# Performance work log

Measured on AMD Instinct MI355X. Metric: run time of the kernel, lower is better.

Reference implementation:

```python
import jax, jax.numpy as jnp
import numpy as np

N_NODES = 8000
N_EDGES = 64000
HEADS = 8
OUT_C = 512
NEG_SLOPE = 0.2
EPS = 1e-16


def setup_inputs() -> dict:
    key = jax.random.key(0)
    ks = jax.random.split(key, 8)
    x = jax.random.normal(ks[0], (N_NODES, 128), dtype=jnp.float32)
    edge_index = jax.random.randint(ks[1], (2, N_EDGES), 0, N_NODES, dtype=jnp.int64)
    W_gat = jax.random.normal(ks[2], (128, HEADS * OUT_C), dtype=jnp.float32) * 0.05
    b_gat = jax.random.normal(ks[3], (HEADS * OUT_C,), dtype=jnp.float32) * 0.05
    att_src = jax.random.normal(ks[4], (HEADS, OUT_C), dtype=jnp.float32) * 0.05
    att_dst = jax.random.normal(ks[5], (HEADS, OUT_C), dtype=jnp.float32) * 0.05
    W_lin = jax.random.normal(ks[6], (HEADS * OUT_C, 512), dtype=jnp.float32) * 0.02
    b_lin = jax.random.normal(ks[7], (512,), dtype=jnp.float32) * 0.02
    return {"x": x, "edge_index": edge_index, "W_gat": W_gat, "b_gat": b_gat,
            "att_src": att_src, "att_dst": att_dst, "W_lin": W_lin, "b_lin": b_lin}


def reference(x, edge_index, W_gat, b_gat, att_src, att_dst, W_lin, b_lin):
    N = x.shape[0]
    # shared linear projection (PyG GATConv single-tensor input): [N, H, C]
    h = (x @ W_gat).reshape(N, HEADS, OUT_C)
    # add self loops (PyG default add_self_loops=True)
    loop = jnp.arange(N, dtype=edge_index.dtype)
    src = jnp.concatenate([edge_index[0], loop])  # source j
    dst = jnp.concatenate([edge_index[1], loop])  # destination i
    # per-node attention logits: [N, H]
    a_src = jnp.einsum('nhc,hc->nh', h, att_src)
    a_dst = jnp.einsum('nhc,hc->nh', h, att_dst)
    # edge logits, leaky relu
    e = jax.nn.leaky_relu(a_src[src] + a_dst[dst], NEG_SLOPE)  # [E, H]
    # softmax over edges sharing a destination
    emax = jax.ops.segment_max(e, dst, num_segments=N)
    ez = jnp.exp(e - emax[dst])
    denom = jax.ops.segment_sum(ez, dst, num_segments=N)
    alpha = ez / (denom[dst] + EPS)  # [E, H]
    # weighted scatter-add of source features
    msg = h[src] * alpha[:, :, None]  # [E, H, C]
    agg = jax.ops.segment_sum(msg, dst, num_segments=N)  # [N, H, C]
    gat_out = agg.reshape(N, HEADS * OUT_C) + b_gat
    return gat_out @ W_lin + b_lin
```

## Files before the change

kernel.cpp:

```cpp
#include <hip/hip_runtime.h>
#include <hip/hip_bf16.h>
#include <type_traits>

#define NN   8000
#define NE   64000
#define NE2  72000
#define NH   8
#define OC   512
#define HC   4096
#define KIN  128
#define NOUT 512
#define YW   1024
#define MAXDEG 64
#define NEG_SLOPE 0.2f

using bf16 = __hip_bfloat16;
typedef float  f32x4  __attribute__((ext_vector_type(4)));
typedef __bf16 bf16x8 __attribute__((ext_vector_type(8)));

static __device__ __forceinline__ void gld_lds16(const bf16* g, bf16* l){
    __builtin_amdgcn_global_load_lds(
        (const __attribute__((address_space(1))) unsigned int*)g,
        (__attribute__((address_space(3))) unsigned int*)l, 16, 0, 0);
}

struct Acc24 { f32x4 a[2][4]; };

static __device__ __forceinline__ void gemm64x128(
    const bf16* __restrict__ A, int lda, const bf16* __restrict__ BT, int ldb,
    int K, bf16* sA, bf16* sB, int tid, Acc24& acc)
{
    const int lane = tid & 63;
    const int w    = tid >> 6;
    const int wm   = w >> 1, wn = w & 1;
    const int m16  = lane & 15, q = lane >> 4;
    const int rA = tid >> 2,  kA = (tid & 3) * 8;
    const int cB0 = tid, cB1 = 256 + tid;
    const int rB0 = cB0 >> 2, kB0 = (cB0 & 3) * 8;
    const int rB1 = cB1 >> 2, kB1 = (cB1 & 3) * 8;
    const size_t gA  = (size_t)rA  * lda + kA;
    const size_t gB0 = (size_t)rB0 * ldb + kB0;
    const size_t gB1 = (size_t)rB1 * ldb + kB1;

    #pragma unroll
    for (int i=0;i<2;++i)
        #pragma unroll
        for (int j=0;j<4;++j)
            #pragma unroll
            for (int r=0;r<4;++r) acc.a[i][j][r] = 0.f;

    gld_lds16(A  + gA,  sA + tid*8);
    gld_lds16(BT + gB0, sB + cB0*8);
    gld_lds16(BT + gB1, sB + cB1*8);
    __syncthreads();

    const int nIter = K / 32;
    for (int it = 0; it < nIter; ++it){
        const int cur = it & 1, nxt = cur ^ 1;
        bf16x8 af[2], bfr[4];
        #pragma unroll
        for (int i=0;i<2;++i)
            af[i]  = *(const bf16x8*)(const void*)(sA + cur*64*32 + ((wm*32 + i*16 + m16)*32 + q*8));
        #pragma unroll
        for (int j=0;j<4;++j)
            bfr[j] = *(const bf16x8*)(const void*)(sB + cur*128*32 + ((wn*64 + j*16 + m16)*32 + q*8));
        if (it + 1 < nIter){
            int ko = (it+1) * 32;
            gld_lds16(A  + gA  + ko, sA + nxt*64*32 + tid*8);
            gld_lds16(BT + gB0 + ko, sB + nxt*128*32 + cB0*8);
            gld_lds16(BT + gB1 + ko, sB + nxt*128*32 + cB1*8);
        }
        #pragma unroll
        for (int i=0;i<2;++i)
            #pragma unroll
            for (int j=0;j<4;++j)
                acc.a[i][j] = __builtin_amdgcn_mfma_f32_16x16x32_bf16(af[i], bfr[j], acc.a[i][j], 0, 0, 0);
        __syncthreads();
    }
}

#define VSRC_NB   128
#define BEFF_BASE 128
#define CNT_BASE  160
#define PHA_NB    442

__global__ __launch_bounds__(256) void k_phaseA(
    const float* __restrict__ b_gat, const float* __restrict__ W_gat,
    const float* __restrict__ att_src, const float* __restrict__ att_dst,
    const float* __restrict__ W_lin,
    const int* __restrict__ eidx,
    bf16* __restrict__ Wg, float* __restrict__ v,
    float* __restrict__ b_eff,
    int* __restrict__ cursors, int* __restrict__ esrc)
{
    const int bid = blockIdx.x;
    const int tid = threadIdx.x;

    if (bid < VSRC_NB){
        int k = bid;
        int lane = tid & 63, g = tid >> 6;
        for (int hh = g; hh < NH; hh += 4){
            const float* wp = W_gat + (size_t)k*HC + hh*OC;
            bf16*        wb = Wg    + (size_t)k*HC + hh*OC;
            const float* as = att_src + hh*OC;
            const float* ad = att_dst + hh*OC;
            float ss = 0.f, sd = 0.f;
            #pragma unroll
            for (int c0=0; c0<OC; c0+=64){
                float wv = wp[c0+lane];
                wb[c0+lane] = __float2bfloat16(wv);
                ss = fmaf(wv, as[c0+lane], ss);
                sd = fmaf(wv, ad[c0+lane], sd);
            }
            #pragma unroll
            for (int off=32; off; off>>=1){
                ss += __shfl_down(ss, off);
                sd += __shfl_down(sd, off);
            }
            if (lane == 0){
                v[k*16 + hh]     = ss;
                v[k*16 + 8 + hh] = sd;
            }
        }
    } else if (bid < CNT_BASE){
        int b = bid - BEFF_BASE;
        int o = tid * 2;
        const float* bg = b_gat + b*128;
        const float* wl = W_lin + (size_t)b*128*NOUT + o;
        float a0 = 0.f, a1 = 0.f;
        #pragma unroll 4
        for (int c=0; c<128; ++c){
            float bv = bg[c];
            float2 wv = *(const float2*)(wl + (size_t)c*NOUT);
            a0 = fmaf(bv, wv.x, a0);
            a1 = fmaf(bv, wv.y, a1);
        }
        atomicAdd(b_eff + o,     a0);
        atomicAdd(b_eff + o + 1, a1);
    } else {
        int e = (bid - CNT_BASE)*256 + tid;
        if (e < NE2){
            int src, dst;
            if (e < NE){ src = eidx[e]; dst = eidx[NE+e]; } else { src = dst = e - NE; }
            int pos = atomicAdd(&cursors[dst], 1);
            if (pos < MAXDEG) esrc[dst*MAXDEG + pos] = src;
        }
    }
}

#define PB_GEMM_NB 64
#define ATT_BASE   64
#define PHB_NB     564

__global__ __launch_bounds__(256) void k_phaseB(
    const bf16* __restrict__ Wg, const float* __restrict__ W_lin,
    bf16* __restrict__ WcT,
    const float* __restrict__ x, const float* __restrict__ v,
    float* __restrict__ a_src, float* __restrict__ a_dst)
{
    __shared__ __align__(16) char smem_raw[16*132*2*4];
    const int bid = blockIdx.x;
    const int tid = threadIdx.x;

    if (bid < PB_GEMM_NB){
        bf16* sA = (bf16*)smem_raw;
        bf16* sB = (bf16*)smem_raw + 64*32;

        const int head = bid >> 3;
        const int rem  = bid & 7;
        const int m0   = (rem >> 2) * 64;
        const int n0   = (rem & 3) * 128;
        const int lane = tid & 63;
        const int w = tid >> 6, wm = w >> 1, wn = w & 1;
        const int m16 = lane & 15, q = lane >> 4;

        const int rA = tid >> 2, kA = (tid & 3) * 8;
        const bf16* Abase = Wg + (size_t)(m0 + rA)*HC + head*OC + kA;

        f32x4 acc[2][4];
        #pragma unroll
        for (int i=0;i<2;++i)
            #pragma unroll
            for (int j=0;j<4;++j)
                #pragma unroll
                for (int r=0;r<4;++r) acc[i][j][r] = 0.f;

        for (int kc = 0; kc < OC; kc += 32){
            __syncthreads();
            gld_lds16(Abase + kc, sA + tid*8);
            #pragma unroll
            for (int u=0; u<4; ++u){
                int idx = tid*4 + u;
                int r    = idx >> 5;
                int gcol = (idx & 31) * 4;
                const float* src = W_lin + (size_t)(head*OC + kc + r)*NOUT + n0 + gcol;
                float4 vv = *(const float4*)src;
                sB[(gcol+0)*32 + r] = __float2bfloat16(vv.x);
                sB[(gcol+1)*32 + r] = __float2bfloat16(vv.y);
                sB[(gcol+2)*32 + r] = __float2bfloat16(vv.z);
                sB[(gcol+3)*32 + r] = __float2bfloat16(vv.w);
            }
            __syncthreads();
            bf16x8 af[2], bfr[4];
            #pragma unroll
            for (int i=0;i<2;++i)
                af[i]  = *(const bf16x8*)(const void*)(sA + ((wm*32 + i*16 + m16)*32 + q*8));
            #pragma unroll
            for (int j=0;j<4;++j)
                bfr[j] = *(const bf16x8*)(const void*)(sB + ((wn*64 + j*16 + m16)*32 + q*8));
            #pragma unroll
            for (int i=0;i<2;++i)
                #pragma unroll
                for (int j=0;j<4;++j)
                    acc[i][j] = __builtin_amdgcn_mfma_f32_16x16x32_bf16(af[i], bfr[j], acc[i][j], 0, 0, 0);
        }

        #pragma unroll
        for (int i=0;i<2;++i){
            int row_base = m0 + wm*32 + i*16 + q*4;
            #pragma unroll
            for (int j=0;j<4;++j){
                int col = n0 + wn*64 + j*16 + m16;
                ushort4 pk;
                bf16 b0 = __float2bfloat16(acc[i][j][0]);
                bf16 b1 = __float2bfloat16(acc[i][j][1]);
                bf16 b2 = __float2bfloat16(acc[i][j][2]);
                bf16 b3 = __float2bfloat16(acc[i][j][3]);
                pk.x = *(unsigned short*)&b0; pk.y = *(unsigned short*)&b1;
                pk.z = *(unsigned short*)&b2; pk.w = *(unsigned short*)&b3;
                *reinterpret_cast<ushort4*>(WcT + (size_t)col*YW + head*KIN + row_base) = pk;
            }
        }
        return;
    }

    float (*xs)[132] = (float(*)[132])smem_raw;
    float (*vt)[132] = (float(*)[132])(smem_raw + 16*132*4);
    int node0 = (bid - ATT_BASE) * 16;
    {
        const float* xg = x + (size_t)node0*KIN;
        int row = tid >> 4, co = (tid & 15) * 8;
        float4 v0 = *(const float4*)(xg + row*KIN + co);
        float4 v1 = *(const float4*)(xg + row*KIN + co + 4);
        *(float4*)&xs[row][co]     = v0;
        *(float4*)&xs[row][co + 4] = v1;
    }
    {
        int base = tid*8;
        #pragma unroll
        for (int j=0;j<8;++j){
            int idx = base + j;
            vt[idx & 15][idx >> 4] = v[idx];
        }
    }
    __syncthreads();
    int ln = tid >> 4, o = tid & 15;
    float acc = 0.f;
    #pragma unroll
    for (int k0=0;k0<KIN;k0+=4){
        float4 xv = *(const float4*)&xs[ln][k0];
        float4 vv = *(const float4*)&vt[o][k0];
        acc += xv.x*vv.x + xv.y*vv.y + xv.z*vv.z + xv.w*vv.w;
    }
    int node = node0 + ln;
    if (o < 8) a_src[node*NH + o]     = acc;
    else       a_dst[node*NH + o - 8] = acc;
}

__global__ __launch_bounds__(256) void k_agg(const int* __restrict__ cnts,
    const int* __restrict__ esrc, const float* __restrict__ a_src,
    const float* __restrict__ a_dst, const float* __restrict__ x,
    bf16* __restrict__ Y)
{
    int node = blockIdx.x*4 + (threadIdx.x >> 6);
    int lane = threadIdx.x & 63;
    int s0 = node*MAXDEG, s1 = s0 + cnts[node];
    int g = lane >> 3, h = lane & 7;
    float adl = a_dst[node*NH + h];
    float m = -1e30f, sum = 0.f;
    for (int e = s0 + g; e < s1; e += 8){
        float l = a_src[esrc[e]*NH + h] + adl;
        l = l > 0.f ? l : NEG_SLOPE*l;
        float mn = fmaxf(m, l);
        sum = sum*__expf(m - mn) + __expf(l - mn);
        m = mn;
    }
    #pragma unroll
    for (int d=8; d<64; d<<=1){
        float mo = __shfl_xor(m, d);
        float so = __shfl_xor(sum, d);
        float mn = fmaxf(m, mo);
        sum = sum*__expf(m - mn) + so*__expf(mo - mn);
        m = mn;
    }
    float inv = 1.f / (sum + 1e-16f);
    float acc[16];
    #pragma unroll
    for (int j=0;j<16;++j) acc[j] = 0.f;
    for (int s=s0; s<s1; ++s){
        int src = esrc[s];
        float wl = 0.f;
        if (lane < 8){
            float l = a_src[src*NH + lane] + adl;
            l = l > 0.f ? l : NEG_SLOPE*l;
            wl = __expf(l - m) * inv;
        }
        float2 xv = *(const float2*)(x + (size_t)src*KIN + lane*2);
        #pragma unroll
        for (int hh=0; hh<8; ++hh){
            float wh = __shfl(wl, hh);
            acc[hh*2]   = fmaf(wh, xv.x, acc[hh*2]);
            acc[hh*2+1] = fmaf(wh, xv.y, acc[hh*2+1]);
        }
    }
    bf16* yp = Y + (size_t)node*YW + lane*2;
    #pragma unroll
    for (int hh=0; hh<8; ++hh){
        bf16 b0 = __float2bfloat16(acc[hh*2]);
        bf16 b1 = __float2bfloat16(acc[hh*2+1]);
        ushort2 pk;
        pk.x = *(unsigned short*)&b0;
        pk.y = *(unsigned short*)&b1;
        *reinterpret_cast<ushort2*>(yp + hh*KIN) = pk;
    }
}

__global__ __launch_bounds__(256) void k_gemm64(
    const bf16* __restrict__ A, const bf16* __restrict__ BT,
    const float* __restrict__ b_eff, const float* __restrict__ b_lin,
    float* __restrict__ C)
{
    __shared__ __align__(16) char smem_raw[24576];
    bf16* sA = (bf16*)smem_raw;
    bf16* sB = (bf16*)(smem_raw + 8192);
    const int tid = threadIdx.x;
    int m0 = blockIdx.x * 64;
    int n0 = blockIdx.y * 128;
    Acc24 acc;
    gemm64x128(A + (size_t)m0*YW, YW, BT + (size_t)n0*YW, YW, YW, sA, sB, tid, acc);
    const int lane = tid & 63;
    const int w = tid >> 6, wm = w >> 1, wn = w & 1;
    const int m16 = lane & 15, q = lane >> 4;
    #pragma unroll
    for (int i=0;i<2;++i){
        int row_base = m0 + wm*32 + i*16 + q*4;
        #pragma unroll
        for (int j=0;j<4;++j){
            int col = n0 + wn*64 + j*16 + m16;
            float bval = b_eff[col] + b_lin[col];
            #pragma unroll
            for (int r=0;r<4;++r)
                C[(size_t)(row_base + r)*NOUT + col] = acc.a[i][j][r] + bval;
        }
    }
}

extern "C" void kernel_launch(void* const* d_in, const int* in_sizes, int n_in,
                              void* d_out, int out_size, void* d_ws, size_t ws_size,
                              hipStream_t stream)
{
    const float* x       = (const float*)d_in[0];
    const int*   eidx    = (const int*)  d_in[1];
    const float* W_gat   = (const float*)d_in[2];
    const float* b_gat   = (const float*)d_in[3];
    const float* att_src = (const float*)d_in[4];
    const float* att_dst = (const float*)d_in[5];
    const float* W_lin   = (const float*)d_in[6];
    const float* b_lin   = (const float*)d_in[7];
    float* out = (float*)d_out;

    char* p = (char*)d_ws;
    auto alloc = [&](size_t bytes){ void* r = (void*)p; p += (bytes + 255) & ~(size_t)255; return r; };
    bf16*  Wg     = (bf16*) alloc((size_t)KIN*HC*2);
    bf16*  WcT    = (bf16*) alloc((size_t)NOUT*YW*2);
    bf16*  Ybuf   = (bf16*) alloc((size_t)NN*YW*2);
    float* v      = (float*)alloc((size_t)KIN*16*4);
    float* a_src  = (float*)alloc((size_t)NN*NH*4);
    float* a_dst  = (float*)alloc((size_t)NN*NH*4);
    int*   esrc   = (int*)  alloc((size_t)NN*MAXDEG*4);
    int*   cursors= (int*)  alloc((size_t)NN*4);
    float* b_eff  = (float*)alloc((size_t)NOUT*4);
    if ((size_t)(p - (char*)d_ws) > ws_size) return;

    hipMemsetAsync(cursors, 0, (size_t)NN*4 + NOUT*4, stream);
    k_phaseA<<<PHA_NB, 256, 0, stream>>>(b_gat, W_gat, att_src, att_dst, W_lin,
                                         eidx, Wg, v, b_eff, cursors, esrc);
    k_phaseB<<<PHB_NB, 256, 0, stream>>>(Wg, W_lin, WcT, x, v, a_src, a_dst);
    k_agg<<<NN/4, 256, 0, stream>>>(cursors, esrc, a_src, a_dst, x, Ybuf);
    k_gemm64<<<dim3(NN/64, NOUT/128), 256, 0, stream>>>(Ybuf, WcT, b_eff, b_lin, out);
}
```

Measured before the change: 151.2 us.

## Fuse all phases into one cooperative persistent kernel with grid syncs

Replaces the memset and four separate kernel launches with a single cooperative kernel of 1024 blocks. The phases run one after another, separated by grid-wide syncs, and blocks loop over the aggregation work. This removes launch gaps and the memset. In exchange it adds grid barrier costs, limits occupancy to what the cooperative launch allows, and forces every phase to use the same 24KB dynamic shared memory. The original multi-kernel path stays as a fallback if the cooperative launch fails, and the degree count is now clamped to MAXDEG.

```diff
diff --git a/kernel.cpp b/kernel.cpp
--- a/kernel.cpp
+++ b/kernel.cpp
@@ -1,6 +1,8 @@
 #include <hip/hip_runtime.h>
+#include <hip/hip_cooperative_groups.h>
 #include <hip/hip_bf16.h>
-#include <type_traits>
+
+namespace cg = cooperative_groups;
 
 #define NN   8000
 #define NE   64000
@@ -14,6 +16,20 @@
 #define MAXDEG 64
 #define NEG_SLOPE 0.2f
 
+#define VSRC_NB   128
+#define BEFF_BASE 128
+#define CNT_BASE  160
+#define PHA_NB    442
+
+#define PB_GEMM_NB 64
+#define ATT_BASE   64
+#define PHB_NB     564
+
+#define AGG_NB    (NN/4)
+#define GEMM_NB   ((NN/64)*(NOUT/128))
+#define GRID_NB   1024
+#define SMEM_BYTES 24576
+
 using bf16 = __hip_bfloat16;
 typedef float  f32x4  __attribute__((ext_vector_type(4)));
 typedef __bf16 bf16x8 __attribute__((ext_vector_type(8)));
@@ -79,23 +95,14 @@
     }
 }
 
-#define VSRC_NB   128
-#define BEFF_BASE 128
-#define CNT_BASE  160
-#define PHA_NB    442
-
-__global__ __launch_bounds__(256) void k_phaseA(
+
+static __device__ __forceinline__ void phaseA_body(int bid, int tid,
     const float* __restrict__ b_gat, const float* __restrict__ W_gat,
     const float* __restrict__ att_src, const float* __restrict__ att_dst,
-    const float* __restrict__ W_lin,
-    const int* __restrict__ eidx,
-    bf16* __restrict__ Wg, float* __restrict__ v,
-    float* __restrict__ b_eff,
+    const float* __restrict__ W_lin, const int* __restrict__ eidx,
+    bf16* __restrict__ Wg, float* __restrict__ v, float* __restrict__ b_eff,
     int* __restrict__ cursors, int* __restrict__ esrc)
 {
-    const int bid = blockIdx.x;
-    const int tid = threadIdx.x;
-
     if (bid < VSRC_NB){
         int k = bid;
         int lane = tid & 63, g = tid >> 6;
@@ -148,23 +155,16 @@
     }
 }
 
-#define PB_GEMM_NB 64
-#define ATT_BASE   64
-#define PHB_NB     564
-
-__global__ __launch_bounds__(256) void k_phaseB(
+static __device__ __forceinline__ void phaseB_body(int bid, int tid,
     const bf16* __restrict__ Wg, const float* __restrict__ W_lin,
     bf16* __restrict__ WcT,
     const float* __restrict__ x, const float* __restrict__ v,
     float* __restrict__ a_src, float* __restrict__ a_dst)
 {
-    __shared__ __align__(16) char smem_raw[16*132*2*4];
-    const int bid = blockIdx.x;
-    const int tid = threadIdx.x;
-
+    extern __shared__ __align__(16) char smem_dyn[];
     if (bid < PB_GEMM_NB){
-        bf16* sA = (bf16*)smem_raw;
-        bf16* sB = (bf16*)smem_raw + 64*32;
+        bf16* sA = (bf16*)smem_dyn;
+        bf16* sB = (bf16*)smem_dyn + 64*32;
 
         const int head = bid >> 3;
         const int rem  = bid & 7;
@@ -234,8 +234,8 @@
         return;
     }
 
-    float (*xs)[132] = (float(*)[132])smem_raw;
-    float (*vt)[132] = (float(*)[132])(smem_raw + 16*132*4);
+    float (*xs)[132] = (float(*)[132])smem_dyn;
+    float (*vt)[132] = (float(*)[132])(smem_dyn + 16*132*4);
     int node0 = (bid - ATT_BASE) * 16;
     {
         const float* xg = x + (size_t)node0*KIN;
@@ -267,14 +267,14 @@
     else       a_dst[node*NH + o - 8] = acc;
 }
 
-__global__ __launch_bounds__(256) void k_agg(const int* __restrict__ cnts,
-    const int* __restrict__ esrc, const float* __restrict__ a_src,
-    const float* __restrict__ a_dst, const float* __restrict__ x,
-    bf16* __restrict__ Y)
-{
-    int node = blockIdx.x*4 + (threadIdx.x >> 6);
-    int lane = threadIdx.x & 63;
-    int s0 = node*MAXDEG, s1 = s0 + cnts[node];
+static __device__ __forceinline__ void agg_body(int bid, int tid,
+    const int* __restrict__ cnts, const int* __restrict__ esrc,
+    const float* __restrict__ a_src, const float* __restrict__ a_dst,
+    const float* __restrict__ x, bf16* __restrict__ Y)
+{
+    int node = bid*4 + (tid >> 6);
+    int lane = tid & 63;
+    int s0 = node*MAXDEG, s1 = s0 + min(cnts[node], MAXDEG);
     int g = lane >> 3, h = lane & 7;
     float adl = a_dst[node*NH + h];
     float m = -1e30f, sum = 0.f;
@@ -325,17 +325,16 @@
     }
 }
 
-__global__ __launch_bounds__(256) void k_gemm64(
+static __device__ __forceinline__ void gemm_body(int bid, int tid,
     const bf16* __restrict__ A, const bf16* __restrict__ BT,
     const float* __restrict__ b_eff, const float* __restrict__ b_lin,
     float* __restrict__ C)
 {
-    __shared__ __align__(16) char smem_raw[24576];
-    bf16* sA = (bf16*)smem_raw;
-    bf16* sB = (bf16*)(smem_raw + 8192);
-    const int tid = threadIdx.x;
-    int m0 = blockIdx.x * 64;
-    int n0 = blockIdx.y * 128;
+    extern __shared__ __align__(16) char smem_dyn[];
+    bf16* sA = (bf16*)smem_dyn;
+    bf16* sB = (bf16*)(smem_dyn + 8192);
+    int m0 = (bid % 125) * 64;
+    int n0 = (bid / 125) * 128;
     Acc24 acc;
     gemm64x128(A + (size_t)m0*YW, YW, BT + (size_t)n0*YW, YW, YW, sA, sB, tid, acc);
     const int lane = tid & 63;
@@ -353,6 +352,79 @@
                 C[(size_t)(row_base + r)*NOUT + col] = acc.a[i][j][r] + bval;
         }
     }
+}
+
+__global__ __launch_bounds__(256, 4) void k_fused(
+    const float* __restrict__ x, const int* __restrict__ eidx,
+    const float* __restrict__ W_gat, const float* __restrict__ b_gat,
+    const float* __restrict__ att_src, const float* __restrict__ att_dst,
+    const float* __restrict__ W_lin, const float* __restrict__ b_lin,
+    float* __restrict__ out,
+    bf16* __restrict__ Wg, bf16* __restrict__ WcT, bf16* __restrict__ Ybuf,
+    float* __restrict__ v, float* __restrict__ a_src, float* __restrict__ a_dst,
+    int* __restrict__ esrc, int* __restrict__ cursors, float* __restrict__ b_eff)
+{
+    cg::grid_group grid = cg::this_grid();
+    const int tid = threadIdx.x;
+    const int gbid = blockIdx.x;
+
+    {
+        int i = gbid*256 + tid;
+        if (i < NN)   cursors[i] = 0;
+        if (i < NOUT) b_eff[i]  = 0.f;
+    }
+    grid.sync();
+
+    if (gbid < PHA_NB)
+        phaseA_body(gbid, tid, b_gat, W_gat, att_src, att_dst, W_lin, eidx,
+                    Wg, v, b_eff, cursors, esrc);
+    grid.sync();
+
+    if (gbid < PHB_NB)
+        phaseB_body(gbid, tid, Wg, W_lin, WcT, x, v, a_src, a_dst);
+    grid.sync();
+
+    for (int bid = gbid; bid < AGG_NB; bid += GRID_NB)
+        agg_body(bid, tid, cursors, esrc, a_src, a_dst, x, Ybuf);
+    grid.sync();
+
+    if (gbid < GEMM_NB)
+        gemm_body(gbid, tid, Ybuf, WcT, b_eff, b_lin, out);
+}
+
+__global__ __launch_bounds__(256) void k_phaseA(
+    const float* __restrict__ b_gat, const float* __restrict__ W_gat,
+    const float* __restrict__ att_src, const float* __restrict__ att_dst,
+    const float* __restrict__ W_lin, const int* __restrict__ eidx,
+    bf16* __restrict__ Wg, float* __restrict__ v, float* __restrict__ b_eff,
+    int* __restrict__ cursors, int* __restrict__ esrc)
+{
+    phaseA_body(blockIdx.x, threadIdx.x, b_gat, W_gat, att_src, att_dst, W_lin,
+                eidx, Wg, v, b_eff, cursors, esrc);
+}
+
+__global__ __launch_bounds__(256) void k_phaseB(
+    const bf16* __restrict__ Wg, const float* __restrict__ W_lin,
+    bf16* __restrict__ WcT, const float* __restrict__ x,
+    const float* __restrict__ v, float* __restrict__ a_src, float* __restrict__ a_dst)
+{
+    phaseB_body(blockIdx.x, threadIdx.x, Wg, W_lin, WcT, x, v, a_src, a_dst);
+}
+
+__global__ __launch_bounds__(256) void k_agg(const int* __restrict__ cnts,
+    const int* __restrict__ esrc, const float* __restrict__ a_src,
+    const float* __restrict__ a_dst, const float* __restrict__ x,
+    bf16* __restrict__ Y)
+{
+    agg_body(blockIdx.x, threadIdx.x, cnts, esrc, a_src, a_dst, x, Y);
+}
+
+__global__ __launch_bounds__(256) void k_gemm64(
+    const bf16* __restrict__ A, const bf16* __restrict__ BT,
+    const float* __restrict__ b_eff, const float* __restrict__ b_lin,
+    float* __restrict__ C)
+{
+    gemm_body(blockIdx.x, threadIdx.x, A, BT, b_eff, b_lin, C);
 }
 
 extern "C" void kernel_launch(void* const* d_in, const int* in_sizes, int n_in,
@@ -382,10 +454,23 @@
     float* b_eff  = (float*)alloc((size_t)NOUT*4);
     if ((size_t)(p - (char*)d_ws) > ws_size) return;
 
-    hipMemsetAsync(cursors, 0, (size_t)NN*4 + NOUT*4, stream);
-    k_phaseA<<<PHA_NB, 256, 0, stream>>>(b_gat, W_gat, att_src, att_dst, W_lin,
-                                         eidx, Wg, v, b_eff, cursors, esrc);
-    k_phaseB<<<PHB_NB, 256, 0, stream>>>(Wg, W_lin, WcT, x, v, a_src, a_dst);
-    k_agg<<<NN/4, 256, 0, stream>>>(cursors, esrc, a_src, a_dst, x, Ybuf);
-    k_gemm64<<<dim3(NN/64, NOUT/128), 256, 0, stream>>>(Ybuf, WcT, b_eff, b_lin, out);
-}
+    void* kargs[] = {
+        (void*)&x, (void*)&eidx, (void*)&W_gat, (void*)&b_gat,
+        (void*)&att_src, (void*)&att_dst, (void*)&W_lin, (void*)&b_lin,
+        (void*)&out,
+        (void*)&Wg, (void*)&WcT, (void*)&Ybuf,
+        (void*)&v, (void*)&a_src, (void*)&a_dst,
+        (void*)&esrc, (void*)&cursors, (void*)&b_eff
+    };
+    hipError_t err = hipLaunchCooperativeKernel(
+        (const void*)k_fused, dim3(GRID_NB), dim3(256), kargs, SMEM_BYTES, stream);
+
+    if (err != hipSuccess){
+        hipMemsetAsync(cursors, 0, (size_t)NN*4 + NOUT*4, stream);
+        k_phaseA<<<PHA_NB, 256, 0, stream>>>(b_gat, W_gat, att_src, att_dst, W_lin,
+                                             eidx, Wg, v, b_eff, cursors, esrc);
+        k_phaseB<<<PHB_NB, 256, SMEM_BYTES, stream>>>(Wg, W_lin, WcT, x, v, a_src, a_dst);
+        k_agg<<<AGG_NB, 256, 0, stream>>>(cursors, esrc, a_src, a_dst, x, Ybuf);
+        k_gemm64<<<GEMM_NB, 256, SMEM_BYTES, stream>>>(Ybuf, WcT, b_eff, b_lin, out);
+    }
+}
```

New measurement: 557.8 us. 269% more time.

## Drop memset, move edge fill and bias partials into phase B, prefetch agg loads

Applied to the files above, without the earlier changes.

Removes the hipMemsetAsync by zeroing the edge cursors inside a block of phase A. Edge bucketing and the folded-bias computation move into phase B, and the bias is written as 16 per-block partials instead of atomics. The epilogue of the final GEMM sums those partials. The aggregation loop software-prefetches the next neighbour's features and logits to hide gather latency, and the per-node count is clamped to MAXDEG. The aim is fewer launches and atomics and better latency hiding, at the cost of 16 extra bias loads per column in the GEMM epilogue.

```diff
diff --git a/kernel.cpp b/kernel.cpp
--- a/kernel.cpp
+++ b/kernel.cpp
@@ -1,6 +1,5 @@
 #include <hip/hip_runtime.h>
 #include <hip/hip_bf16.h>
-#include <type_traits>
 
 #define NN   8000
 #define NE   64000
@@ -14,6 +13,15 @@
 #define MAXDEG 64
 #define NEG_SLOPE 0.2f
 
+#define VSRC_NB   128
+#define PHA_NB    129
+
+#define PB_GEMM_NB 64
+#define FILL_BASE  64
+#define BEFF_BASE  346
+#define ATT_BASE   362
+#define PHB_NB     862
+
 using bf16 = __hip_bfloat16;
 typedef float  f32x4  __attribute__((ext_vector_type(4)));
 typedef __bf16 bf16x8 __attribute__((ext_vector_type(8)));
@@ -79,19 +87,11 @@
     }
 }
 
-#define VSRC_NB   128
-#define BEFF_BASE 128
-#define CNT_BASE  160
-#define PHA_NB    442
-
 __global__ __launch_bounds__(256) void k_phaseA(
-    const float* __restrict__ b_gat, const float* __restrict__ W_gat,
+    const float* __restrict__ W_gat,
     const float* __restrict__ att_src, const float* __restrict__ att_dst,
-    const float* __restrict__ W_lin,
-    const int* __restrict__ eidx,
     bf16* __restrict__ Wg, float* __restrict__ v,
-    float* __restrict__ b_eff,
-    int* __restrict__ cursors, int* __restrict__ esrc)
+    int* __restrict__ cursors)
 {
     const int bid = blockIdx.x;
     const int tid = threadIdx.x;
@@ -122,39 +122,19 @@
                 v[k*16 + 8 + hh] = sd;
             }
         }
-    } else if (bid < CNT_BASE){
-        int b = bid - BEFF_BASE;
-        int o = tid * 2;
-        const float* bg = b_gat + b*128;
-        const float* wl = W_lin + (size_t)b*128*NOUT + o;
-        float a0 = 0.f, a1 = 0.f;
-        #pragma unroll 4
-        for (int c=0; c<128; ++c){
-            float bv = bg[c];
-            float2 wv = *(const float2*)(wl + (size_t)c*NOUT);
-            a0 = fmaf(bv, wv.x, a0);
-            a1 = fmaf(bv, wv.y, a1);
-        }
-        atomicAdd(b_eff + o,     a0);
-        atomicAdd(b_eff + o + 1, a1);
     } else {
-        int e = (bid - CNT_BASE)*256 + tid;
-        if (e < NE2){
-            int src, dst;
-            if (e < NE){ src = eidx[e]; dst = eidx[NE+e]; } else { src = dst = e - NE; }
-            int pos = atomicAdd(&cursors[dst], 1);
-            if (pos < MAXDEG) esrc[dst*MAXDEG + pos] = src;
-        }
-    }
-}
-
-#define PB_GEMM_NB 64
-#define ATT_BASE   64
-#define PHB_NB     564
+        for (int i = tid*4; i < NN; i += 1024){
+            int4 z; z.x = z.y = z.z = z.w = 0;
+            *reinterpret_cast<int4*>(cursors + i) = z;
+        }
+    }
+}
 
 __global__ __launch_bounds__(256) void k_phaseB(
     const bf16* __restrict__ Wg, const float* __restrict__ W_lin,
-    bf16* __restrict__ WcT,
+    const float* __restrict__ b_gat, const int* __restrict__ eidx,
+    bf16* __restrict__ WcT, float* __restrict__ beff_part,
+    int* __restrict__ cursors, int* __restrict__ esrc,
     const float* __restrict__ x, const float* __restrict__ v,
     float* __restrict__ a_src, float* __restrict__ a_dst)
 {
@@ -234,6 +214,35 @@
         return;
     }
 
+    if (bid < BEFF_BASE){
+        int e = (bid - FILL_BASE)*256 + tid;
+        if (e < NE2){
+            int src, dst;
+            if (e < NE){ src = eidx[e]; dst = eidx[NE+e]; } else { src = dst = e - NE; }
+            int pos = atomicAdd(&cursors[dst], 1);
+            if (pos < MAXDEG) esrc[dst*MAXDEG + pos] = src;
+        }
+        return;
+    }
+
+    if (bid < ATT_BASE){
+        int b = bid - BEFF_BASE;
+        int o = tid * 2;
+        const float* bg = b_gat + b*256;
+        const float* wl = W_lin + (size_t)b*256*NOUT + o;
+        float a0 = 0.f, a1 = 0.f;
+        #pragma unroll 4
+        for (int r=0; r<256; ++r){
+            float bv = bg[r];
+            float2 wv = *(const float2*)(wl + (size_t)r*NOUT);
+            a0 = fmaf(bv, wv.x, a0);
+            a1 = fmaf(bv, wv.y, a1);
+        }
+        beff_part[b*NOUT + o]     = a0;
+        beff_part[b*NOUT + o + 1] = a1;
+        return;
+    }
+
     float (*xs)[132] = (float(*)[132])smem_raw;
     float (*vt)[132] = (float(*)[132])(smem_raw + 16*132*4);
     int node0 = (bid - ATT_BASE) * 16;
@@ -274,7 +283,7 @@
 {
     int node = blockIdx.x*4 + (threadIdx.x >> 6);
     int lane = threadIdx.x & 63;
-    int s0 = node*MAXDEG, s1 = s0 + cnts[node];
+    int s0 = node*MAXDEG, s1 = s0 + min(cnts[node], MAXDEG);
     int g = lane >> 3, h = lane & 7;
     float adl = a_dst[node*NH + h];
     float m = -1e30f, sum = 0.f;
@@ -297,15 +306,24 @@
     float acc[16];
     #pragma unroll
     for (int j=0;j<16;++j) acc[j] = 0.f;
-    for (int s=s0; s<s1; ++s){
-        int src = esrc[s];
+
+    int src_n = esrc[s0];
+    float2 xv_n = *(const float2*)(x + (size_t)src_n*KIN + lane*2);
+    float al_n = (lane < 8) ? a_src[src_n*NH + lane] : 0.f;
+    for (int s = s0; s < s1; ++s){
+        float2 xv = xv_n;
+        float al = al_n;
+        if (s + 1 < s1){
+            int sn = esrc[s+1];
+            xv_n = *(const float2*)(x + (size_t)sn*KIN + lane*2);
+            al_n = (lane < 8) ? a_src[sn*NH + lane] : 0.f;
+        }
         float wl = 0.f;
         if (lane < 8){
-            float l = a_src[src*NH + lane] + adl;
+            float l = al + adl;
             l = l > 0.f ? l : NEG_SLOPE*l;
             wl = __expf(l - m) * inv;
         }
-        float2 xv = *(const float2*)(x + (size_t)src*KIN + lane*2);
         #pragma unroll
         for (int hh=0; hh<8; ++hh){
             float wh = __shfl(wl, hh);
@@ -327,7 +345,7 @@
 
 __global__ __launch_bounds__(256) void k_gemm64(
     const bf16* __restrict__ A, const bf16* __restrict__ BT,
-    const float* __restrict__ b_eff, const float* __restrict__ b_lin,
+    const float* __restrict__ beff_part, const float* __restrict__ b_lin,
     float* __restrict__ C)
 {
     __shared__ __align__(16) char smem_raw[24576];
@@ -342,12 +360,14 @@
     const int w = tid >> 6, wm = w >> 1, wn = w & 1;
     const int m16 = lane & 15, q = lane >> 4;
     #pragma unroll
-    for (int i=0;i<2;++i){
-        int row_base = m0 + wm*32 + i*16 + q*4;
-        #pragma unroll
-        for (int j=0;j<4;++j){
-            int col = n0 + wn*64 + j*16 + m16;
-            float bval = b_eff[col] + b_lin[col];
+    for (int j=0;j<4;++j){
+        int col = n0 + wn*64 + j*16 + m16;
+        float bval = b_lin[col];
+        #pragma unroll
+        for (int p=0;p<16;++p) bval += beff_part[p*NOUT + col];
+        #pragma unroll
+        for (int i=0;i<2;++i){
+            int row_base = m0 + wm*32 + i*16 + q*4;
             #pragma unroll
             for (int r=0;r<4;++r)
                 C[(size_t)(row_base + r)*NOUT + col] = acc.a[i][j][r] + bval;
@@ -371,21 +391,20 @@
 
     char* p = (char*)d_ws;
     auto alloc = [&](size_t bytes){ void* r = (void*)p; p += (bytes + 255) & ~(size_t)255; return r; };
-    bf16*  Wg     = (bf16*) alloc((size_t)KIN*HC*2);
-    bf16*  WcT    = (bf16*) alloc((size_t)NOUT*YW*2);
-    bf16*  Ybuf   = (bf16*) alloc((size_t)NN*YW*2);
-    float* v      = (float*)alloc((size_t)KIN*16*4);
-    float* a_src  = (float*)alloc((size_t)NN*NH*4);
-    float* a_dst  = (float*)alloc((size_t)NN*NH*4);
-    int*   esrc   = (int*)  alloc((size_t)NN*MAXDEG*4);
-    int*   cursors= (int*)  alloc((size_t)NN*4);
-    float* b_eff  = (float*)alloc((size_t)NOUT*4);
+    bf16*  Wg        = (bf16*) alloc((size_t)KIN*HC*2);
+    bf16*  WcT       = (bf16*) alloc((size_t)NOUT*YW*2);
+    bf16*  Ybuf      = (bf16*) alloc((size_t)NN*YW*2);
+    float* v         = (float*)alloc((size_t)KIN*16*4);
+    float* a_src     = (float*)alloc((size_t)NN*NH*4);
+    float* a_dst     = (float*)alloc((size_t)NN*NH*4);
+    int*   esrc      = (int*)  alloc((size_t)NN*MAXDEG*4);
+    int*   cursors   = (int*)  alloc((size_t)NN*4);
+    float* beff_part = (float*)alloc((size_t)16*NOUT*4);
     if ((size_t)(p - (char*)d_ws) > ws_size) return;
 
-    hipMemsetAsync(cursors, 0, (size_t)NN*4 + NOUT*4, stream);
-    k_phaseA<<<PHA_NB, 256, 0, stream>>>(b_gat, W_gat, att_src, att_dst, W_lin,
-                                         eidx, Wg, v, b_eff, cursors, esrc);
-    k_phaseB<<<PHB_NB, 256, 0, stream>>>(Wg, W_lin, WcT, x, v, a_src, a_dst);
+    k_phaseA<<<PHA_NB, 256, 0, stream>>>(W_gat, att_src, att_dst, Wg, v, cursors);
+    k_phaseB<<<PHB_NB, 256, 0, stream>>>(Wg, W_lin, b_gat, eidx, WcT, beff_part,
+                                         cursors, esrc, x, v, a_src, a_dst);
     k_agg<<<NN/4, 256, 0, stream>>>(cursors, esrc, a_src, a_dst, x, Ybuf);
-    k_gemm64<<<dim3(NN/64, NOUT/128), 256, 0, stream>>>(Ybuf, WcT, b_eff, b_lin, out);
-}
+    k_gemm64<<<dim3(NN/64, NOUT/128), 256, 0, stream>>>(Ybuf, WcT, beff_part, b_lin, out);
+}
```

Result: faster. 139.9 us (-7.5%).
